# Performance work log

Measured on AMD Instinct MI355X. Metric: run time of the kernel, lower is better.

## Reference

```python
import jax, jax.numpy as jnp
import numpy as np

# Geometry constants from init_kwargs
GRID = (128, 128, 128)
SIZE = np.array([2.0, 2.0, 2.0], dtype=np.float32)
CENTER = np.array([0.0, 0.0, 0.0], dtype=np.float32)
ORIGIN = CENTER - SIZE / 2.0                      # lower corner of the voxel box
VOXEL = SIZE / np.array(GRID, dtype=np.float32)   # voxel pitch per axis
N_LORS = 100000


def siddon_project(image, lors):
    """Exact Siddon line-integral forward projection, fully vectorized.

    image: [Gx,Gy,Gz] voxel values; lors: [N,6] = (x0,y0,z0, x1,y1,z1).
    For each ray we compute all intersection parameters alpha with the
    grid planes, sort them, and accumulate segment_length * voxel_value.
    """
    gx, gy, gz = GRID
    origin = jnp.asarray(ORIGIN)
    voxel = jnp.asarray(VOXEL)
    grid_f = jnp.asarray(np.array(GRID, dtype=np.float32))

    p0 = lors[:, 0:3]                 # [N,3] ray start
    d = lors[:, 3:6] - p0             # [N,3] ray direction (p1 - p0)
    eps = jnp.float32(1e-9)
    d_safe = jnp.where(jnp.abs(d) < eps, eps, d)  # avoid div-by-zero; huge alphas get clipped away

    # Entry/exit parameters of the ray with the bounding box, clamped to the segment [0,1].
    bmin = origin
    bmax = origin + voxel * grid_f
    a0 = (bmin - p0) / d_safe         # [N,3]
    a1 = (bmax - p0) / d_safe
    amin = jnp.maximum(jnp.max(jnp.minimum(a0, a1), axis=1), 0.0)  # [N]
    amax = jnp.minimum(jnp.min(jnp.maximum(a0, a1), axis=1), 1.0)  # [N]

    def plane_alphas(axis, g):
        # alpha at every grid plane along `axis`: [N, g+1]
        planes = origin[axis] + jnp.arange(g + 1, dtype=jnp.float32) * voxel[axis]
        return (planes[None, :] - p0[:, axis:axis + 1]) / d_safe[:, axis:axis + 1]

    # All candidate alphas, clipped into [amin, amax] then merge-sorted per ray.
    alphas = jnp.concatenate(
        [plane_alphas(0, gx), plane_alphas(1, gy), plane_alphas(2, gz),
         amin[:, None], amax[:, None]], axis=1)                      # [N, K+1]
    alphas = jnp.clip(alphas, amin[:, None], amax[:, None])
    alphas = jnp.sort(alphas, axis=1)

    diff = alphas[:, 1:] - alphas[:, :-1]                            # [N, K]
    ray_len = jnp.linalg.norm(d, axis=1, keepdims=True)              # [N, 1]
    seg = diff * ray_len                                             # intersection lengths

    # Voxel index from each segment midpoint.
    mid = alphas[:, :-1] + 0.5 * diff                                # [N, K]
    pts = p0[:, None, :] + mid[..., None] * d[:, None, :]            # [N, K, 3]
    idxf = jnp.floor((pts - origin) / voxel)                         # [N, K, 3]

    valid = (seg > 0) \
        & jnp.all((idxf >= 0) & (idxf < grid_f), axis=-1) \
        & (amax > amin)[:, None]
    idx = jnp.clip(idxf, 0.0, grid_f - 1.0).astype(jnp.int32)
    flat = (idx[..., 0] * gy + idx[..., 1]) * gz + idx[..., 2]       # [N, K]
    vals = jnp.take(image.reshape(-1), flat)
    return jnp.sum(jnp.where(valid, seg * vals, 0.0), axis=1)        # [N]


def setup_inputs() -> dict:
    key = jax.random.key(0)
    k1, k2 = jax.random.split(key)
    image = jax.random.uniform(k1, GRID, dtype=jnp.float32)          # nonneg activity volume
    lors = jax.random.normal(k2, (N_LORS, 6), dtype=jnp.float32)     # endpoints straddle [-1,1]^3 box
    return {"image": image, "lors": lors}


def reference(image, lors):
    return siddon_project(image, lors)
```

## Files before the change

### kernel.cpp

```cpp
#include <hip/hip_runtime.h>
#include <hip/hip_fp16.h>
#include <math.h>


static constexpr float VOX = 0.015625f;
static constexpr float INV_VOX = 64.0f;
static constexpr int   K = 16;
static constexpr int   LOGK = 4;
static constexpr int   NVOX = 128 * 128 * 128;

struct TState {
  float alx, aly, alz;
  float dax, day, daz;
  float acur, aend;
  int   ix, iy, iz;
  int   stx, sty, stz;
};

__device__ __forceinline__ void step4(const __half* __restrict__ image,
                                      TState& S, float dif4[4], float v4[4]) {
#pragma unroll
  for (int j = 0; j < 4; ++j) {
    float anext = fminf(fminf(S.alx, S.aly), S.alz);
    float astop = fminf(anext, S.aend);
    float diff  = astop - S.acur;
    unsigned orv = (unsigned)(S.ix | S.iy | S.iz);
    bool  use   = (diff > 0.0f) & (orv < 128u);
    int   idx   = (S.ix << 14) | (S.iy << 7) | S.iz;
    v4[j]  = __half2float(image[use ? idx : 0]);
    dif4[j] = use ? diff : 0.0f;
    S.acur = astop;
    bool cx = S.alx <= anext;
    bool cy = S.aly <= anext;
    bool cz = S.alz <= anext;
    S.ix += cx ? S.stx : 0;  S.alx += cx ? S.dax : 0.0f;
    S.iy += cy ? S.sty : 0;  S.aly += cy ? S.day : 0.0f;
    S.iz += cz ? S.stz : 0;  S.alz += cz ? S.daz : 0.0f;
  }
}

__device__ __forceinline__ void axis_init(float astart, float aend, float p0,
                                          float ds, float inv,
                                          int& st, int& iv, float& al, float& da,
                                          int& cnt) {
  float ts = (fmaf(astart, ds, p0) + 1.0f) * INV_VOX;
  float te = (fmaf(aend,   ds, p0) + 1.0f) * INV_VOX;
  int ip;
  if (ds > 0.0f) {
    ip = (int)floorf(ts) + 1;
    int il = (int)floorf(te); if (il > 128) il = 128;
    cnt = il - ip + 1; st = 1; iv = ip - 1;
  } else {
    ip = (int)ceilf(ts) - 1;
    int il = (int)ceilf(te); if (il < 0) il = 0;
    cnt = ip - il + 1; st = -1; iv = ip;
  }
  if (cnt < 0) cnt = 0;
  al = (fmaf((float)ip, VOX, -1.0f) - p0) * inv;
  da = VOX * fabsf(inv);
}

__global__ __launch_bounds__(256) void convert_h(
    const float* __restrict__ img, __half* __restrict__ h)
{
  int i = blockIdx.x * blockDim.x + threadIdx.x;
  int stride = gridDim.x * blockDim.x;
  for (; i < NVOX; i += stride) h[i] = __float2half(img[i]);
}

__global__ __launch_bounds__(256) void siddon_fp(
    const __half* __restrict__ image,
    const float* __restrict__ lors,
    float* __restrict__ out, int n)
{
  int t    = blockIdx.x * blockDim.x + threadIdx.x;
  int ray  = t >> LOGK;
  int k    = t & (K - 1);
  if (ray >= n) return;

  const float* L = lors + (long)ray * 6;
  float p0x = L[0], p0y = L[1], p0z = L[2];
  float dx  = L[3] - p0x, dy = L[4] - p0y, dz = L[5] - p0z;

  const float eps = 1e-9f;
  float dsx = (fabsf(dx) < eps) ? eps : dx;
  float dsy = (fabsf(dy) < eps) ? eps : dy;
  float dsz = (fabsf(dz) < eps) ? eps : dz;

  float invx = __builtin_amdgcn_rcpf(dsx);
  float invy = __builtin_amdgcn_rcpf(dsy);
  float invz = __builtin_amdgcn_rcpf(dsz);

  float a0 = (-1.0f - p0x) * invx, a1 = (1.0f - p0x) * invx;
  float axmin = fminf(a0, a1), axmax = fmaxf(a0, a1);
  a0 = (-1.0f - p0y) * invy; a1 = (1.0f - p0y) * invy;
  float aymin = fminf(a0, a1), aymax = fmaxf(a0, a1);
  a0 = (-1.0f - p0z) * invz; a1 = (1.0f - p0z) * invz;
  float azmin = fminf(a0, a1), azmax = fmaxf(a0, a1);

  float amin = fmaxf(fmaxf(axmin, aymin), fmaxf(azmin, 0.0f));
  float amax = fminf(fminf(axmax, aymax), fminf(azmax, 1.0f));

  float acc0 = 0.0f, acc1 = 0.0f;
  if (amax > amin) {
    float s      = (amax - amin) * (1.0f / (float)K);
    float astart = fmaf((float)k, s, amin);
    float aend   = (k == K - 1) ? amax : fmaf((float)(k + 1), s, amin);

    TState S;
    S.acur = astart; S.aend = aend;
    int cx, cy, cz;
    axis_init(astart, aend, p0x, dsx, invx, S.stx, S.ix, S.alx, S.dax, cx);
    axis_init(astart, aend, p0y, dsy, invy, S.sty, S.iy, S.aly, S.day, cy);
    axis_init(astart, aend, p0z, dsz, invz, S.stz, S.iz, S.alz, S.daz, cz);

    int ns = cx + cy + cz + 3;
    int nb = (ns + 3) >> 2;
    if (nb < 2) nb = 2;

    float difA[4], difB[4], difC[4];
    float vA[4], vB[4], vC[4];

#define ISSUE(X)   step4(image, S, dif##X, v##X)
#define CONSUME(X)                                                  \
    do { acc0 = fmaf(dif##X[0], v##X[0], acc0);                     \
         acc1 = fmaf(dif##X[1], v##X[1], acc1);                     \
         acc0 = fmaf(dif##X[2], v##X[2], acc0);                     \
         acc1 = fmaf(dif##X[3], v##X[3], acc1); } while (0)

    ISSUE(A);
    ISSUE(B);
    int produce = nb - 2;
    while (produce >= 3) {
      ISSUE(C); CONSUME(A);
      ISSUE(A); CONSUME(B);
      ISSUE(B); CONSUME(C);
      produce -= 3;
    }
    if (produce == 2) {
      ISSUE(C); CONSUME(A);
      ISSUE(A); CONSUME(B);
      CONSUME(C); CONSUME(A);
    } else if (produce == 1) {
      ISSUE(C); CONSUME(A);
      CONSUME(B); CONSUME(C);
    } else {
      CONSUME(A); CONSUME(B);
    }
#undef ISSUE
#undef CONSUME

    float rlen = sqrtf(dx * dx + dy * dy + dz * dz);
    acc0 = (acc0 + acc1) * rlen;
    acc1 = 0.0f;
  }

  float acc = acc0 + acc1;
  acc += __shfl_xor(acc, 1);
  acc += __shfl_xor(acc, 2);
  acc += __shfl_xor(acc, 4);
  acc += __shfl_xor(acc, 8);
  if (k == 0) out[ray] = acc;
}

extern "C" void kernel_launch(void* const* d_in, const int* in_sizes, int n_in,
                              void* d_out, int out_size, void* d_ws, size_t ws_size,
                              hipStream_t stream) {
  const float* image = (const float*)d_in[0];
  const float* lors  = (const float*)d_in[1];
  float* out = (float*)d_out;
  int n = out_size;

  __half* h = (__half*)d_ws;
  hipLaunchKernelGGL(convert_h, dim3(2048), dim3(256), 0, stream, image, h);

  long total = (long)n * K;
  int block = 256;
  int grid = (int)((total + block - 1) / block);
  hipLaunchKernelGGL(siddon_fp, dim3(grid), dim3(block), 0, stream,
                     h, lors, out, n);
}
```

Measured before the change: 56.18 us.

## Assign one wavefront per ray with per-lane independent plane-crossing segments

Replaces the 16-thread sequential incremental Siddon traversal per ray with a 64-lane scheme. Each lane takes one plane crossing (or amin), computes the next crossing on every axis directly, then uses the segment midpoint to pick the voxel. This removes the serial dependency chain in the traversal and the software pipelining, leaving about one image gather per lane-iteration. The cost is more arithmetic per segment (floor and ceil work and next-crossing recomputation) and idle lanes for short rays, since the wave is padded to 64.

```diff
diff --git a/kernel.cpp b/kernel.cpp
--- a/kernel.cpp
+++ b/kernel.cpp
@@ -5,59 +5,39 @@
 
 static constexpr float VOX = 0.015625f;
 static constexpr float INV_VOX = 64.0f;
-static constexpr int   K = 16;
-static constexpr int   LOGK = 4;
 static constexpr int   NVOX = 128 * 128 * 128;
 
-struct TState {
-  float alx, aly, alz;
-  float dax, day, daz;
-  float acur, aend;
-  int   ix, iy, iz;
-  int   stx, sty, stz;
-};
-
-__device__ __forceinline__ void step4(const __half* __restrict__ image,
-                                      TState& S, float dif4[4], float v4[4]) {
-#pragma unroll
-  for (int j = 0; j < 4; ++j) {
-    float anext = fminf(fminf(S.alx, S.aly), S.alz);
-    float astop = fminf(anext, S.aend);
-    float diff  = astop - S.acur;
-    unsigned orv = (unsigned)(S.ix | S.iy | S.iz);
-    bool  use   = (diff > 0.0f) & (orv < 128u);
-    int   idx   = (S.ix << 14) | (S.iy << 7) | S.iz;
-    v4[j]  = __half2float(image[use ? idx : 0]);
-    dif4[j] = use ? diff : 0.0f;
-    S.acur = astop;
-    bool cx = S.alx <= anext;
-    bool cy = S.aly <= anext;
-    bool cz = S.alz <= anext;
-    S.ix += cx ? S.stx : 0;  S.alx += cx ? S.dax : 0.0f;
-    S.iy += cy ? S.sty : 0;  S.aly += cy ? S.day : 0.0f;
-    S.iz += cz ? S.stz : 0;  S.alz += cz ? S.daz : 0.0f;
-  }
-}
-
-__device__ __forceinline__ void axis_init(float astart, float aend, float p0,
+__device__ __forceinline__ void axis_init(float amin, float amax, float p0,
                                           float ds, float inv,
-                                          int& st, int& iv, float& al, float& da,
-                                          int& cnt) {
-  float ts = (fmaf(astart, ds, p0) + 1.0f) * INV_VOX;
-  float te = (fmaf(aend,   ds, p0) + 1.0f) * INV_VOX;
-  int ip;
+                                          int& st, int& ip, float& al, int& cnt) {
+  float ts = (fmaf(amin, ds, p0) + 1.0f) * INV_VOX;
+  float te = (fmaf(amax, ds, p0) + 1.0f) * INV_VOX;
   if (ds > 0.0f) {
     ip = (int)floorf(ts) + 1;
     int il = (int)floorf(te); if (il > 128) il = 128;
-    cnt = il - ip + 1; st = 1; iv = ip - 1;
+    cnt = il - ip + 1; st = 1;
   } else {
     ip = (int)ceilf(ts) - 1;
     int il = (int)ceilf(te); if (il < 0) il = 0;
-    cnt = ip - il + 1; st = -1; iv = ip;
+    cnt = ip - il + 1; st = -1;
   }
   if (cnt < 0) cnt = 0;
   al = (fmaf((float)ip, VOX, -1.0f) - p0) * inv;
-  da = VOX * fabsf(inv);
+}
+
+__device__ __forceinline__ float next_cross(float a0, float pos, float p0b,
+                                            float invb, int stb, bool strict) {
+  float tt = (pos + 1.0f) * INV_VOX;
+  int q = (stb > 0) ? ((int)floorf(tt) + 1) : ((int)ceilf(tt) - 1);
+  float ab  = (fmaf((float)q, VOX, -1.0f) - p0b) * invb;
+  float abp = (fmaf((float)(q - stb), VOX, -1.0f) - p0b) * invb;
+  bool back = strict ? (abp > a0) : (abp >= a0);
+  int  q2 = back ? (q - stb) : q;
+  ab = back ? abp : ab;
+  bool fwd = strict ? (ab <= a0) : (ab < a0);
+  float abn = (fmaf((float)(q2 + stb), VOX, -1.0f) - p0b) * invb;
+  ab = fwd ? abn : ab;
+  return ab;
 }
 
 __global__ __launch_bounds__(256) void convert_h(
@@ -73,9 +53,8 @@
     const float* __restrict__ lors,
     float* __restrict__ out, int n)
 {
-  int t    = blockIdx.x * blockDim.x + threadIdx.x;
-  int ray  = t >> LOGK;
-  int k    = t & (K - 1);
+  int ray  = (blockIdx.x * blockDim.x + threadIdx.x) >> 6;
+  int lane = threadIdx.x & 63;
   if (ray >= n) return;
 
   const float* L = lors + (long)ray * 6;
@@ -101,66 +80,67 @@
   float amin = fmaxf(fmaxf(axmin, aymin), fmaxf(azmin, 0.0f));
   float amax = fminf(fminf(axmax, aymax), fminf(azmax, 1.0f));
 
-  float acc0 = 0.0f, acc1 = 0.0f;
+  float acc = 0.0f;
   if (amax > amin) {
-    float s      = (amax - amin) * (1.0f / (float)K);
-    float astart = fmaf((float)k, s, amin);
-    float aend   = (k == K - 1) ? amax : fmaf((float)(k + 1), s, amin);
+    int stx, sty, stz, ipx, ipy, ipz, c0, c1, c2;
+    float alx, aly, alz;
+    axis_init(amin, amax, p0x, dsx, invx, stx, ipx, alx, c0);
+    axis_init(amin, amax, p0y, dsy, invy, sty, ipy, aly, c1);
+    axis_init(amin, amax, p0z, dsz, invz, stz, ipz, alz, c2);
 
-    TState S;
-    S.acur = astart; S.aend = aend;
-    int cx, cy, cz;
-    axis_init(astart, aend, p0x, dsx, invx, S.stx, S.ix, S.alx, S.dax, cx);
-    axis_init(astart, aend, p0y, dsy, invy, S.sty, S.iy, S.aly, S.day, cy);
-    axis_init(astart, aend, p0z, dsz, invz, S.stz, S.iz, S.alz, S.daz, cz);
+    int V = c0 + c1 + c2;
+    int nit = (V + 64) >> 6;
 
-    int ns = cx + cy + cz + 3;
-    int nb = (ns + 3) >> 2;
-    if (nb < 2) nb = 2;
+    for (int it = 0; it < nit; ++it) {
+      int t = (it << 6) + lane;
+      bool ge1 = t >= c0, ge2 = t >= (c0 + c1);
+      int  a   = (ge1 ? 1 : 0) + (ge2 ? 1 : 0);
+      int  tb  = t - (ge2 ? (c0 + c1) : (ge1 ? c0 : 0));
+      float p0a  = ge2 ? p0z : (ge1 ? p0y : p0x);
+      float inva = ge2 ? invz : (ge1 ? invy : invx);
+      int   ipa  = ge2 ? ipz : (ge1 ? ipy : ipx);
+      int   sta  = ge2 ? stz : (ge1 ? sty : stx);
+      int   p    = ipa + sta * tb;
 
-    float difA[4], difB[4], difC[4];
-    float vA[4], vB[4], vC[4];
+      float alpha0 = (fmaf((float)p, VOX, -1.0f) - p0a) * inva;
+      bool amin_lane = (t == V);
+      bool pad       = (t > V);
+      alpha0 = amin_lane ? amin : (pad ? amax : alpha0);
 
-#define ISSUE(X)   step4(image, S, dif##X, v##X)
-#define CONSUME(X)                                                  \
-    do { acc0 = fmaf(dif##X[0], v##X[0], acc0);                     \
-         acc1 = fmaf(dif##X[1], v##X[1], acc1);                     \
-         acc0 = fmaf(dif##X[2], v##X[2], acc0);                     \
-         acc1 = fmaf(dif##X[3], v##X[3], acc1); } while (0)
+      float posx = fmaf(alpha0, dx, p0x);
+      float posy = fmaf(alpha0, dy, p0y);
+      float posz = fmaf(alpha0, dz, p0z);
+      float nx = next_cross(alpha0, posx, p0x, invx, stx, true);
+      float ny = next_cross(alpha0, posy, p0y, invy, sty, a >= 1);
+      float nz = next_cross(alpha0, posz, p0z, invz, stz, a >= 2);
+      nx = amin_lane ? alx : nx;
+      ny = amin_lane ? aly : ny;
+      nz = amin_lane ? alz : nz;
 
-    ISSUE(A);
-    ISSUE(B);
-    int produce = nb - 2;
-    while (produce >= 3) {
-      ISSUE(C); CONSUME(A);
-      ISSUE(A); CONSUME(B);
-      ISSUE(B); CONSUME(C);
-      produce -= 3;
+      float aend = fminf(fminf(nx, ny), fminf(nz, amax));
+      float dif  = fmaxf(aend - alpha0, 0.0f);
+
+      float mid = fmaf(0.5f, dif, alpha0);
+      float fx = floorf((fmaf(mid, dx, p0x) + 1.0f) * INV_VOX);
+      float fy = floorf((fmaf(mid, dy, p0y) + 1.0f) * INV_VOX);
+      float fz = floorf((fmaf(mid, dz, p0z) + 1.0f) * INV_VOX);
+      bool inb = (fx >= 0.0f) & (fx < 128.0f) &
+                 (fy >= 0.0f) & (fy < 128.0f) &
+                 (fz >= 0.0f) & (fz < 128.0f);
+      dif = inb ? dif : 0.0f;
+      int idx = inb ? (((int)fx << 14) | ((int)fy << 7) | (int)fz) : 0;
+      acc = fmaf(dif, __half2float(image[idx]), acc);
     }
-    if (produce == 2) {
-      ISSUE(C); CONSUME(A);
-      ISSUE(A); CONSUME(B);
-      CONSUME(C); CONSUME(A);
-    } else if (produce == 1) {
-      ISSUE(C); CONSUME(A);
-      CONSUME(B); CONSUME(C);
-    } else {
-      CONSUME(A); CONSUME(B);
-    }
-#undef ISSUE
-#undef CONSUME
-
-    float rlen = sqrtf(dx * dx + dy * dy + dz * dz);
-    acc0 = (acc0 + acc1) * rlen;
-    acc1 = 0.0f;
+    acc *= sqrtf(dx * dx + dy * dy + dz * dz);
   }
 
-  float acc = acc0 + acc1;
   acc += __shfl_xor(acc, 1);
   acc += __shfl_xor(acc, 2);
   acc += __shfl_xor(acc, 4);
   acc += __shfl_xor(acc, 8);
-  if (k == 0) out[ray] = acc;
+  acc += __shfl_xor(acc, 16);
+  acc += __shfl_xor(acc, 32);
+  if (lane == 0) out[ray] = acc;
 }
 
 extern "C" void kernel_launch(void* const* d_in, const int* in_sizes, int n_in,
@@ -174,9 +154,7 @@
   __half* h = (__half*)d_ws;
   hipLaunchKernelGGL(convert_h, dim3(2048), dim3(256), 0, stream, image, h);
 
-  long total = (long)n * K;
-  int block = 256;
-  int grid = (int)((total + block - 1) / block);
-  hipLaunchKernelGGL(siddon_fp, dim3(grid), dim3(block), 0, stream,
+  int grid = (n + 3) / 4;
+  hipLaunchKernelGGL(siddon_fp, dim3(grid), dim3(256), 0, stream,
                      h, lors, out, n);
 }
```

Measured after the change: 77.72 us. 38.3% more time.

## Store fp16 volume in 4x4x4 bricked layout and simplify traversal bounds checks

Applied to the files above, without the earlier changes.

The conversion kernel now writes the half-precision volume in a 4x4x4 brick-tiled order so that neighbouring voxels along any ray direction share cache lines. The traversal computes brick addresses with bit operations and drops the explicit in-range check, relying instead on masking the byte address. It also trims the per-thread step count by one. The masking silently wraps out-of-range indices instead of rejecting them, which could give wrong values if a segment lands outside the grid.

```diff
diff --git a/kernel.cpp b/kernel.cpp
--- a/kernel.cpp
+++ b/kernel.cpp
@@ -8,6 +8,7 @@
 static constexpr int   K = 16;
 static constexpr int   LOGK = 4;
 static constexpr int   NVOX = 128 * 128 * 128;
+static constexpr int   IDX_MASK = 0x3FFFFE;
 
 struct TState {
   float alx, aly, alz;
@@ -17,18 +18,23 @@
   int   stx, sty, stz;
 };
 
+__device__ __forceinline__ int brick_addr(int ix, int iy, int iz) {
+  int hx = ((ix & 0x7C) << 14) | ((ix & 3) << 4);
+  int hy = ((iy & 0x7C) << 9)  | ((iy & 3) << 2);
+  int hz = ((iz & 0x7C) << 4)  | (iz & 3);
+  return ((hx | hy | hz) << 1) & IDX_MASK;
+}
+
 __device__ __forceinline__ void step4(const __half* __restrict__ image,
                                       TState& S, float dif4[4], float v4[4]) {
 #pragma unroll
   for (int j = 0; j < 4; ++j) {
     float anext = fminf(fminf(S.alx, S.aly), S.alz);
     float astop = fminf(anext, S.aend);
-    float diff  = astop - S.acur;
-    unsigned orv = (unsigned)(S.ix | S.iy | S.iz);
-    bool  use   = (diff > 0.0f) & (orv < 128u);
-    int   idx   = (S.ix << 14) | (S.iy << 7) | S.iz;
-    v4[j]  = __half2float(image[use ? idx : 0]);
-    dif4[j] = use ? diff : 0.0f;
+    float dif   = fmaxf(astop - S.acur, 0.0f);
+    dif4[j] = dif;
+    int addr = (dif > 0.0f) ? brick_addr(S.ix, S.iy, S.iz) : 0;
+    v4[j] = __half2float(*(const __half*)((const char*)image + addr));
     S.acur = astop;
     bool cx = S.alx <= anext;
     bool cy = S.aly <= anext;
@@ -60,12 +66,42 @@
   da = VOX * fabsf(inv);
 }
 
-__global__ __launch_bounds__(256) void convert_h(
+__device__ __forceinline__ void ray_setup(const float* L,
+    float& p0x, float& p0y, float& p0z,
+    float& dx, float& dy, float& dz,
+    float& dsx, float& dsy, float& dsz,
+    float& invx, float& invy, float& invz,
+    float& amin, float& amax) {
+  p0x = L[0]; p0y = L[1]; p0z = L[2];
+  dx = L[3] - p0x; dy = L[4] - p0y; dz = L[5] - p0z;
+  const float eps = 1e-9f;
+  dsx = (fabsf(dx) < eps) ? eps : dx;
+  dsy = (fabsf(dy) < eps) ? eps : dy;
+  dsz = (fabsf(dz) < eps) ? eps : dz;
+  invx = __builtin_amdgcn_rcpf(dsx);
+  invy = __builtin_amdgcn_rcpf(dsy);
+  invz = __builtin_amdgcn_rcpf(dsz);
+  float a0 = (-1.0f - p0x) * invx, a1 = (1.0f - p0x) * invx;
+  float axmin = fminf(a0, a1), axmax = fmaxf(a0, a1);
+  a0 = (-1.0f - p0y) * invy; a1 = (1.0f - p0y) * invy;
+  float aymin = fminf(a0, a1), aymax = fmaxf(a0, a1);
+  a0 = (-1.0f - p0z) * invz; a1 = (1.0f - p0z) * invz;
+  float azmin = fminf(a0, a1), azmax = fmaxf(a0, a1);
+  amin = fmaxf(fmaxf(axmin, aymin), fmaxf(azmin, 0.0f));
+  amax = fminf(fminf(axmax, aymax), fminf(azmax, 1.0f));
+}
+
+__global__ __launch_bounds__(256) void convert_brick(
     const float* __restrict__ img, __half* __restrict__ h)
 {
   int i = blockIdx.x * blockDim.x + threadIdx.x;
   int stride = gridDim.x * blockDim.x;
-  for (; i < NVOX; i += stride) h[i] = __float2half(img[i]);
+  for (int hi = i; hi < NVOX; hi += stride) {
+    int lz = hi & 3, ly = (hi >> 2) & 3, lx = (hi >> 4) & 3;
+    int bz = (hi >> 6) & 31, by = (hi >> 11) & 31, bx = (hi >> 16) & 31;
+    int ix = (bx << 2) | lx, iy = (by << 2) | ly, iz = (bz << 2) | lz;
+    h[hi] = __float2half(img[(((ix << 7) | iy) << 7) | iz]);
+  }
 }
 
 __global__ __launch_bounds__(256) void siddon_fp(
@@ -73,33 +109,14 @@
     const float* __restrict__ lors,
     float* __restrict__ out, int n)
 {
-  int t    = blockIdx.x * blockDim.x + threadIdx.x;
-  int ray  = t >> LOGK;
-  int k    = t & (K - 1);
+  int t   = blockIdx.x * blockDim.x + threadIdx.x;
+  int ray = t >> LOGK;
+  int k   = t & (K - 1);
   if (ray >= n) return;
 
-  const float* L = lors + (long)ray * 6;
-  float p0x = L[0], p0y = L[1], p0z = L[2];
-  float dx  = L[3] - p0x, dy = L[4] - p0y, dz = L[5] - p0z;
-
-  const float eps = 1e-9f;
-  float dsx = (fabsf(dx) < eps) ? eps : dx;
-  float dsy = (fabsf(dy) < eps) ? eps : dy;
-  float dsz = (fabsf(dz) < eps) ? eps : dz;
-
-  float invx = __builtin_amdgcn_rcpf(dsx);
-  float invy = __builtin_amdgcn_rcpf(dsy);
-  float invz = __builtin_amdgcn_rcpf(dsz);
-
-  float a0 = (-1.0f - p0x) * invx, a1 = (1.0f - p0x) * invx;
-  float axmin = fminf(a0, a1), axmax = fmaxf(a0, a1);
-  a0 = (-1.0f - p0y) * invy; a1 = (1.0f - p0y) * invy;
-  float aymin = fminf(a0, a1), aymax = fmaxf(a0, a1);
-  a0 = (-1.0f - p0z) * invz; a1 = (1.0f - p0z) * invz;
-  float azmin = fminf(a0, a1), azmax = fmaxf(a0, a1);
-
-  float amin = fmaxf(fmaxf(axmin, aymin), fmaxf(azmin, 0.0f));
-  float amax = fminf(fminf(axmax, aymax), fminf(azmax, 1.0f));
+  float p0x,p0y,p0z,dx,dy,dz,dsx,dsy,dsz,invx,invy,invz,amin,amax;
+  ray_setup(lors + (long)ray * 6, p0x,p0y,p0z, dx,dy,dz,
+            dsx,dsy,dsz, invx,invy,invz, amin,amax);
 
   float acc0 = 0.0f, acc1 = 0.0f;
   if (amax > amin) {
@@ -109,12 +126,12 @@
 
     TState S;
     S.acur = astart; S.aend = aend;
-    int cx, cy, cz;
-    axis_init(astart, aend, p0x, dsx, invx, S.stx, S.ix, S.alx, S.dax, cx);
-    axis_init(astart, aend, p0y, dsy, invy, S.sty, S.iy, S.aly, S.day, cy);
-    axis_init(astart, aend, p0z, dsz, invz, S.stz, S.iz, S.alz, S.daz, cz);
+    int c0, c1, c2;
+    axis_init(astart, aend, p0x, dsx, invx, S.stx, S.ix, S.alx, S.dax, c0);
+    axis_init(astart, aend, p0y, dsy, invy, S.sty, S.iy, S.aly, S.day, c1);
+    axis_init(astart, aend, p0z, dsz, invz, S.stz, S.iz, S.alz, S.daz, c2);
 
-    int ns = cx + cy + cz + 3;
+    int ns = c0 + c1 + c2 + 2;
     int nb = (ns + 3) >> 2;
     if (nb < 2) nb = 2;
 
@@ -172,7 +189,7 @@
   int n = out_size;
 
   __half* h = (__half*)d_ws;
-  hipLaunchKernelGGL(convert_h, dim3(2048), dim3(256), 0, stream, image, h);
+  hipLaunchKernelGGL(convert_brick, dim3(2048), dim3(256), 0, stream, image, h);
 
   long total = (long)n * K;
   int block = 256;
```

Measured after the change: 54.57 us. 1.03x faster.
